# Kernel optimization log

Hardware: AMD Instinct MI355X
Metric: run time of the kernel (lower is better)

The kernel has to match this reference:

```python
import jax, jax.numpy as jnp
import numpy as np

EPS = 1e-7
LN_EPS = 1e-5

# Lorentz model, points represented by spatial coords x in R^dim; time coord t = sqrt(K + ||x||^2), K = 1/c.

def log_map_zero(x, c):
    K = 1.0 / c
    sqrtK = jnp.sqrt(K)
    xnorm = jnp.linalg.norm(x, axis=-1, keepdims=True)
    t = jnp.sqrt(K + xnorm * xnorm)
    theta = jnp.arccosh(jnp.maximum(t / sqrtK, 1.0 + EPS))
    return sqrtK * theta * x / jnp.maximum(xnorm, EPS)


def exp_map_zero(v, c):
    K = 1.0 / c
    sqrtK = jnp.sqrt(K)
    vnorm = jnp.linalg.norm(v, axis=-1, keepdims=True)
    return sqrtK * jnp.sinh(vnorm / sqrtK) * v / jnp.maximum(vnorm, EPS)


def layer_norm(x, gamma, beta):
    mu = jnp.mean(x, axis=-1, keepdims=True)
    var = jnp.mean((x - mu) ** 2, axis=-1, keepdims=True)
    return (x - mu) * jax.lax.rsqrt(var + LN_EPS) * gamma + beta


def setup_inputs() -> dict:
    key = jax.random.key(0)
    N, D, E, L = 50000, 128, 800000, 2
    ks = jax.random.split(key, 8)
    x_hyp = jax.random.normal(ks[0], (N, D), dtype=jnp.float32)
    edge_index = jax.random.randint(ks[1], (2, E), 0, N, dtype=jnp.int64)
    W = jax.random.normal(ks[2], (L, D, D), dtype=jnp.float32) / np.sqrt(D)
    b = jnp.zeros((L, D), dtype=jnp.float32)
    gamma = jnp.ones((L, D), dtype=jnp.float32)
    beta = jnp.zeros((L, D), dtype=jnp.float32)
    curv = jnp.ones((L,), dtype=jnp.float32)
    return {"x_hyp": x_hyp, "edge_index": edge_index, "W": W, "b": b,
            "gamma": gamma, "beta": beta, "curv": curv}


def reference(x_hyp, edge_index, W, b, gamma, beta, curv):
    N = x_hyp.shape[0]
    L = W.shape[0]
    src, dst = edge_index[0], edge_index[1]
    # in-degree counts for mean aggregation (clamped to avoid div by 0)
    counts = jax.ops.segment_sum(jnp.ones_like(dst, dtype=x_hyp.dtype), dst, num_segments=N)
    counts = jnp.maximum(counts, 1.0)[:, None]
    x = x_hyp
    for l in range(L):
        # curvature treated as constant (torch uses .item())
        c = jax.lax.stop_gradient(jnp.clip(curv[l], 0.1, 10.0))
        x_tan = log_map_zero(x, c)                      # [N, D]
        x_lin = x_tan @ W[l].T + b[l]                   # [N, D]
        msgs = x_lin[src]                               # [E, D] gather
        agg = jax.ops.segment_sum(msgs, dst, num_segments=N) / counts  # scatter-mean
        x_tan_out = layer_norm(x_tan + agg, gamma[l], beta[l])  # dropout in eval mode
        x = exp_map_zero(x_tan_out, c)
    return x
```

## Files before the change

kernel.cpp:

```cpp
#include <hip/hip_runtime.h>
#include <hip/hip_bf16.h>

typedef __attribute__((ext_vector_type(4))) float f32x4;
typedef __attribute__((ext_vector_type(8))) short bf16x8;

constexpr int D = 128;
constexpr int SB = 256;
constexpr int K4CAP = 8192;
#define FEPS 1e-7f
#define FLN_EPS 1e-5f

__device__ __forceinline__ float groupReduceSum16(float x) {
#pragma unroll
  for (int off = 1; off < 16; off <<= 1) x += __shfl_xor(x, off, 64);
  return x;
}

__device__ __forceinline__ unsigned short f2bf(float x) {
  unsigned int u = __float_as_uint(x);
  u += 0x7fffu + ((u >> 16) & 1u);
  return (unsigned short)(u >> 16);
}

__device__ __forceinline__ unsigned int pack2(float a, float b) {
  return (unsigned int)f2bf(a) | ((unsigned int)f2bf(b) << 16);
}

__device__ __forceinline__ void acc8(float* a, uint4 u) {
  a[0] += __uint_as_float(u.x << 16);
  a[1] += __uint_as_float(u.x & 0xffff0000u);
  a[2] += __uint_as_float(u.y << 16);
  a[3] += __uint_as_float(u.y & 0xffff0000u);
  a[4] += __uint_as_float(u.z << 16);
  a[5] += __uint_as_float(u.z & 0xffff0000u);
  a[6] += __uint_as_float(u.w << 16);
  a[7] += __uint_as_float(u.w & 0xffff0000u);
}


__global__ __launch_bounds__(1024) void k1_hist(const int* __restrict__ dst,
                                                int* __restrict__ bh, int E, int NB, int chunk) {
  __shared__ int h[256];
  int tid = threadIdx.x;
  if (tid < 256) h[tid] = 0;
  __syncthreads();
  int e0 = blockIdx.x * chunk;
  int e1 = min(e0 + chunk, E);
  for (int e = e0 + tid; e < e1; e += 1024) atomicAdd(&h[dst[e] >> 8], 1);
  __syncthreads();
  if (tid < NB) bh[tid * SB + blockIdx.x] = h[tid];
}

__global__ __launch_bounds__(1024) void k2_scan(int* __restrict__ bh,
                                                int* __restrict__ bucket_base, int NB, int E) {
  __shared__ int bsum[256];
  int tid = threadIdx.x, lane = tid & 63, wv = tid >> 6;
  for (int bin = wv; bin < NB; bin += 16) {
    int carry = 0;
    int* row = bh + bin * SB;
#pragma unroll
    for (int sgm = 0; sgm < 4; ++sgm) {
      int v = row[sgm * 64 + lane];
      int x = v;
#pragma unroll
      for (int off = 1; off < 64; off <<= 1) {
        int t = __shfl_up(x, off, 64);
        if (lane >= off) x += t;
      }
      row[sgm * 64 + lane] = carry + x - v;
      carry += __shfl(x, 63, 64);
    }
    if (lane == 0) bsum[bin] = carry;
  }
  __syncthreads();
  if (wv == 0) {
    int carry = 0;
    for (int base = 0; base < NB; base += 64) {
      int v = (base + lane < NB) ? bsum[base + lane] : 0;
      int x = v;
#pragma unroll
      for (int off = 1; off < 64; off <<= 1) {
        int t = __shfl_up(x, off, 64);
        if (lane >= off) x += t;
      }
      if (base + lane < NB) {
        int excl = carry + x - v;
        bsum[base + lane] = excl;
        bucket_base[base + lane] = excl;
      }
      carry += __shfl(x, 63, 64);
    }
    if (lane == 0) bucket_base[NB] = E;
  }
  __syncthreads();
  for (int bin = wv; bin < NB; bin += 16) {
    int bb = bsum[bin];
    int* row = bh + bin * SB;
    for (int s = lane; s < SB; s += 64) row[s] += bb;
  }
}

__global__ __launch_bounds__(1024) void k3_scatter(const int* __restrict__ src,
                                                   const int* __restrict__ dst,
                                                   const int* __restrict__ bh,
                                                   unsigned int* __restrict__ ebuf, int E,
                                                   int NB, int chunk) {
  __shared__ int base[256];
  __shared__ int cur[256];
  int tid = threadIdx.x;
  if (tid < 256) {
    base[tid] = (tid < NB) ? bh[tid * SB + blockIdx.x] : 0;
    cur[tid] = 0;
  }
  __syncthreads();
  int e0 = blockIdx.x * chunk;
  int e1 = min(e0 + chunk, E);
  for (int e = e0 + tid; e < e1; e += 1024) {
    int d = dst[e];
    int s = src[e];
    int bin = d >> 8;
    int r = atomicAdd(&cur[bin], 1);
    ebuf[base[bin] + r] = (unsigned int)(s & 0xffff) | ((unsigned int)(d & 255) << 16);
  }
}

__global__ __launch_bounds__(1024) void k4_csr(const unsigned int* __restrict__ ebuf,
                                               const int* __restrict__ bucket_base,
                                               int* __restrict__ rowptr,
                                               unsigned short* __restrict__ col, int N, int NB,
                                               int E) {
  __shared__ unsigned int stash[K4CAP];
  __shared__ int hist[256];
  __shared__ int cur[256];
  int b = blockIdx.x, tid = threadIdx.x;
  int e0 = bucket_base[b], e1 = bucket_base[b + 1];
  int cnt = e1 - e0;
  if (tid < 256) {
    hist[tid] = 0;
    cur[tid] = 0;
  }
  __syncthreads();
  for (int i = tid; i < cnt; i += 1024) {
    unsigned int u = ebuf[e0 + i];
    if (i < K4CAP) stash[i] = u;
    atomicAdd(&hist[u >> 16], 1);
  }
  __syncthreads();
  int lane = tid & 63;
  if (tid < 64) {
    int carry = 0;
#pragma unroll
    for (int sgm = 0; sgm < 4; ++sgm) {
      int v = hist[sgm * 64 + lane];
      int x = v;
#pragma unroll
      for (int off = 1; off < 64; off <<= 1) {
        int t = __shfl_up(x, off, 64);
        if (lane >= off) x += t;
      }
      hist[sgm * 64 + lane] = carry + x - v;
      carry += __shfl(x, 63, 64);
    }
  }
  __syncthreads();
  int node0 = b << 8;
  if (tid < 256 && node0 + tid < N) rowptr[node0 + tid] = e0 + hist[tid];
  if (b == 0 && tid == 0) rowptr[N] = E;
  for (int i = tid; i < cnt; i += 1024) {
    unsigned int u = (i < K4CAP) ? stash[i] : ebuf[e0 + i];
    int slot = u >> 16;
    int r = atomicAdd(&cur[slot], 1);
    col[e0 + hist[slot] + r] = (unsigned short)(u & 0xffff);
  }
}


template <int FIRST>
__global__ __launch_bounds__(256) void gemm_kernel(const float* __restrict__ xf,
                                                   const unsigned short* __restrict__ A,
                                                   const float* __restrict__ Wf,
                                                   const float* __restrict__ bias,
                                                   const float* __restrict__ curv, int l,
                                                   unsigned short* __restrict__ xt,
                                                   unsigned short* __restrict__ xl, int N) {
  __shared__ unsigned short Wlds[128 * 128];
  const float* Wp = Wf + (size_t)l * D * D;
  for (int idx = threadIdx.x; idx < 2048; idx += 256) {
    int lanei = idx & 63, kbt = idx >> 6;
    int kb = kbt & 3, tcol = kbt >> 2;
    int g = lanei >> 4, r = lanei & 15;
    const float* s = Wp + (size_t)(tcol * 16 + r) * D + kb * 32 + g * 8;
    float4 f0 = *reinterpret_cast<const float4*>(s);
    float4 f1 = *reinterpret_cast<const float4*>(s + 4);
    uint4 u;
    u.x = pack2(f0.x, f0.y);
    u.y = pack2(f0.z, f0.w);
    u.z = pack2(f1.x, f1.y);
    u.w = pack2(f1.z, f1.w);
    *reinterpret_cast<uint4*>(&Wlds[idx * 8]) = u;
  }
  __syncthreads();
  int lane = threadIdx.x & 63;
  int trow = blockIdx.x * 4 + (threadIdx.x >> 6);
  int n0 = trow * 16;
  if (n0 >= N) return;
  int g = lane >> 4, r = lane & 15;
  int ar = n0 + r;
  if (ar > N - 1) ar = N - 1;

  bf16x8 af[4];
  if (FIRST) {
    float c = fminf(fmaxf(curv[l], 0.1f), 10.0f);
    float K = 1.0f / c, sqrtK = sqrtf(K);
    float4 fa[4][2];
    float ss = 0.f;
#pragma unroll
    for (int kb = 0; kb < 4; ++kb) {
      const float4* xr = reinterpret_cast<const float4*>(xf + (size_t)ar * D + kb * 32 + g * 8);
      fa[kb][0] = xr[0];
      fa[kb][1] = xr[1];
      ss += fa[kb][0].x * fa[kb][0].x + fa[kb][0].y * fa[kb][0].y +
            fa[kb][0].z * fa[kb][0].z + fa[kb][0].w * fa[kb][0].w;
      ss += fa[kb][1].x * fa[kb][1].x + fa[kb][1].y * fa[kb][1].y +
            fa[kb][1].z * fa[kb][1].z + fa[kb][1].w * fa[kb][1].w;
    }
    ss += __shfl_xor(ss, 16, 64);
    ss += __shfl_xor(ss, 32, 64);
    float xnorm = sqrtf(ss);
    float t = sqrtf(K + ss);
    float theta = acoshf(fmaxf(t / sqrtK, 1.0f + FEPS));
    float scale = sqrtK * theta / fmaxf(xnorm, FEPS);
#pragma unroll
    for (int kb = 0; kb < 4; ++kb) {
      union { bf16x8 v; uint4 u; } cv;
      cv.u.x = pack2(fa[kb][0].x * scale, fa[kb][0].y * scale);
      cv.u.y = pack2(fa[kb][0].z * scale, fa[kb][0].w * scale);
      cv.u.z = pack2(fa[kb][1].x * scale, fa[kb][1].y * scale);
      cv.u.w = pack2(fa[kb][1].z * scale, fa[kb][1].w * scale);
      af[kb] = cv.v;
      *reinterpret_cast<uint4*>(xt + (size_t)ar * D + kb * 32 + g * 8) = cv.u;
    }
  } else {
#pragma unroll
    for (int kb = 0; kb < 4; ++kb)
      af[kb] = *reinterpret_cast<const bf16x8*>(A + (size_t)ar * D + kb * 32 + g * 8);
  }

  int colj = lane & 15, rb = (lane >> 4) * 4;
#pragma unroll
  for (int tcol = 0; tcol < 8; ++tcol) {
    f32x4 acc = {0.f, 0.f, 0.f, 0.f};
#pragma unroll
    for (int kb = 0; kb < 4; ++kb) {
      bf16x8 bfm = *reinterpret_cast<const bf16x8*>(&Wlds[((tcol * 4 + kb) * 64 + lane) * 8]);
      acc = __builtin_amdgcn_mfma_f32_16x16x32_bf16(af[kb], bfm, acc, 0, 0, 0);
    }
    float bv = bias[l * D + tcol * 16 + colj];
#pragma unroll
    for (int i = 0; i < 4; ++i) {
      int row = n0 + rb + i;
      if (row < N) xl[(size_t)row * D + tcol * 16 + colj] = f2bf(acc[i] + bv);
    }
  }
}


template <int MODE>
__global__ __launch_bounds__(256) void agg_kernel(const unsigned short* __restrict__ xl,
                                                  unsigned short* __restrict__ xt,
                                                  const int* __restrict__ rowptr,
                                                  const unsigned short* __restrict__ col,
                                                  const float* __restrict__ gamma,
                                                  const float* __restrict__ beta,
                                                  const float* __restrict__ curv, int l,
                                                  float* __restrict__ out, int N) {
  int tid = threadIdx.x;
  int lane = tid & 63;
  int gl = lane & 15, g = lane >> 4;
  int wid = tid >> 6;
  int node = blockIdx.x * 16 + wid * 4 + g;
  bool active = node < N;
  int nd = active ? node : N - 1;

  float c = fminf(fmaxf(curv[l], 0.1f), 10.0f);
  float K = 1.0f / c, sqrtK = sqrtf(K);

  int e0 = rowptr[nd], e1 = rowptr[nd + 1];
  int deg = e1 - e0;
  const unsigned short* cb = col + e0;

  float a[8], a2[8], a3[8], a4[8];
#pragma unroll
  for (int j = 0; j < 8; ++j) { a[j] = 0.f; a2[j] = 0.f; a3[j] = 0.f; a4[j] = 0.f; }

  const uint4* xlp = reinterpret_cast<const uint4*>(xl);
  for (int base = 0; base < deg; base += 16) {
    int cidx = (base + gl < deg) ? (int)cb[base + gl] : 0;
    int m = deg - base;
    if (m > 16) m = 16;
    int k = 0;
    for (; k + 4 <= m; k += 4) {
      int s0 = __shfl(cidx, g * 16 + k, 64);
      int s1 = __shfl(cidx, g * 16 + k + 1, 64);
      int s2 = __shfl(cidx, g * 16 + k + 2, 64);
      int s3 = __shfl(cidx, g * 16 + k + 3, 64);
      uint4 u0 = xlp[(size_t)s0 * 16 + gl];
      uint4 u1 = xlp[(size_t)s1 * 16 + gl];
      uint4 u2 = xlp[(size_t)s2 * 16 + gl];
      uint4 u3 = xlp[(size_t)s3 * 16 + gl];
      acc8(a, u0);
      acc8(a2, u1);
      acc8(a3, u2);
      acc8(a4, u3);
    }
    for (; k < m; ++k) {
      int s0 = __shfl(cidx, g * 16 + k, 64);
      uint4 u0 = xlp[(size_t)s0 * 16 + gl];
      acc8(a, u0);
    }
  }
#pragma unroll
  for (int j = 0; j < 8; ++j) a[j] += a2[j] + a3[j] + a4[j];

  float inv = 1.f / fmaxf((float)deg, 1.f);
  uint4 ut = reinterpret_cast<const uint4*>(xt)[(size_t)nd * 16 + gl];
  float v[8];
  v[0] = __uint_as_float(ut.x << 16) + a[0] * inv;
  v[1] = __uint_as_float(ut.x & 0xffff0000u) + a[1] * inv;
  v[2] = __uint_as_float(ut.y << 16) + a[2] * inv;
  v[3] = __uint_as_float(ut.y & 0xffff0000u) + a[3] * inv;
  v[4] = __uint_as_float(ut.z << 16) + a[4] * inv;
  v[5] = __uint_as_float(ut.z & 0xffff0000u) + a[5] * inv;
  v[6] = __uint_as_float(ut.w << 16) + a[6] * inv;
  v[7] = __uint_as_float(ut.w & 0xffff0000u) + a[7] * inv;

  float s1 = 0.f, s2 = 0.f;
#pragma unroll
  for (int j = 0; j < 8; ++j) { s1 += v[j]; s2 += v[j] * v[j]; }
  s1 = groupReduceSum16(s1);
  s2 = groupReduceSum16(s2);
  float mu = s1 * (1.f / 128.f);
  float var = fmaxf(s2 * (1.f / 128.f) - mu * mu, 0.f);
  float rstd = rsqrtf(var + FLN_EPS);

  float4 gm0 = *reinterpret_cast<const float4*>(gamma + l * D + gl * 8);
  float4 gm1 = *reinterpret_cast<const float4*>(gamma + l * D + gl * 8 + 4);
  float4 bt0 = *reinterpret_cast<const float4*>(beta + l * D + gl * 8);
  float4 bt1 = *reinterpret_cast<const float4*>(beta + l * D + gl * 8 + 4);
  float y[8];
  y[0] = (v[0] - mu) * rstd * gm0.x + bt0.x;
  y[1] = (v[1] - mu) * rstd * gm0.y + bt0.y;
  y[2] = (v[2] - mu) * rstd * gm0.z + bt0.z;
  y[3] = (v[3] - mu) * rstd * gm0.w + bt0.w;
  y[4] = (v[4] - mu) * rstd * gm1.x + bt1.x;
  y[5] = (v[5] - mu) * rstd * gm1.y + bt1.y;
  y[6] = (v[6] - mu) * rstd * gm1.z + bt1.z;
  y[7] = (v[7] - mu) * rstd * gm1.w + bt1.w;

  float ss = 0.f;
#pragma unroll
  for (int j = 0; j < 8; ++j) ss += y[j] * y[j];
  ss = groupReduceSum16(ss);
  float vn = sqrtf(ss);
  float sc = sqrtK * sinhf(vn / sqrtK) / fmaxf(vn, FEPS);

  if (MODE == 0) {
    if (active) {
      float4 o0, o1;
      o0.x = y[0] * sc; o0.y = y[1] * sc; o0.z = y[2] * sc; o0.w = y[3] * sc;
      o1.x = y[4] * sc; o1.y = y[5] * sc; o1.z = y[6] * sc; o1.w = y[7] * sc;
      float4* op = reinterpret_cast<float4*>(out + (size_t)node * D + gl * 8);
      op[0] = o0;
      op[1] = o1;
    }
  } else {
    float xn = sqrtK * sinhf(vn / sqrtK);
    float c2 = fminf(fmaxf(curv[l + 1], 0.1f), 10.0f);
    float K2 = 1.0f / c2, sqrtK2 = sqrtf(K2);
    float t2 = sqrtf(K2 + xn * xn);
    float theta = acoshf(fmaxf(t2 / sqrtK2, 1.0f + FEPS));
    float sc2 = sqrtK2 * theta / fmaxf(xn, FEPS);
    float st = sc * sc2;
    if (active) {
      uint4 w;
      w.x = pack2(y[0] * st, y[1] * st);
      w.y = pack2(y[2] * st, y[3] * st);
      w.z = pack2(y[4] * st, y[5] * st);
      w.w = pack2(y[6] * st, y[7] * st);
      reinterpret_cast<uint4*>(xt)[(size_t)node * 16 + gl] = w;
    }
  }
}


extern "C" void kernel_launch(void* const* d_in, const int* in_sizes, int n_in,
                              void* d_out, int out_size, void* d_ws, size_t ws_size,
                              hipStream_t stream) {
  const float* x_hyp = (const float*)d_in[0];
  const int* edge = (const int*)d_in[1];
  const float* W = (const float*)d_in[2];
  const float* b = (const float*)d_in[3];
  const float* gamma = (const float*)d_in[4];
  const float* beta = (const float*)d_in[5];
  const float* curv = (const float*)d_in[6];
  float* out = (float*)d_out;
  int N = in_sizes[0] / D;
  int E = in_sizes[1] / 2;
  int L = in_sizes[6];
  const int* src = edge;
  const int* dst = edge + E;

  char* p = (char*)d_ws;
  auto alloc = [&](size_t bytes) {
    char* r = p;
    p += (bytes + 255) & ~(size_t)255;
    return r;
  };
  int NB = (N + 255) >> 8;
  int chunk = (E + SB - 1) / SB;

  int* bh = (int*)alloc((size_t)256 * SB * 4);
  int* bucket_base = (int*)alloc((size_t)(NB + 1) * 4);
  unsigned int* ebuf = (unsigned int*)alloc((size_t)E * 4);
  int* rowptr = (int*)alloc((size_t)(N + 1) * 4);
  unsigned short* colp = (unsigned short*)alloc((size_t)E * 2);
  unsigned short* xt16 = (unsigned short*)alloc((size_t)N * D * 2);
  unsigned short* xl16 = (unsigned short*)alloc((size_t)N * D * 2);

  k1_hist<<<SB, 1024, 0, stream>>>(dst, bh, E, NB, chunk);
  k2_scan<<<1, 1024, 0, stream>>>(bh, bucket_base, NB, E);
  k3_scatter<<<SB, 1024, 0, stream>>>(src, dst, bh, ebuf, E, NB, chunk);
  k4_csr<<<NB, 1024, 0, stream>>>(ebuf, bucket_base, rowptr, colp, N, NB, E);

  int gblocks = ((N + 15) / 16 + 3) / 4;
  for (int l = 0; l < L; ++l) {
    if (l == 0) {
      gemm_kernel<1><<<gblocks, 256, 0, stream>>>(x_hyp, nullptr, W, b, curv, l, xt16, xl16, N);
    } else {
      gemm_kernel<0><<<gblocks, 256, 0, stream>>>(nullptr, xt16, W, b, curv, l, nullptr, xl16, N);
    }
    if (l < L - 1) {
      agg_kernel<1><<<(N + 15) / 16, 256, 0, stream>>>(xl16, xt16, rowptr, colp, gamma, beta,
                                                       curv, l, out, N);
    } else {
      agg_kernel<0><<<(N + 15) / 16, 256, 0, stream>>>(xl16, xt16, rowptr, colp, gamma, beta,
                                                       curv, l, out, N);
    }
  }
}
```

Measured before the change: 163.1 us.

## Fuse degree histogram with layer-0 GEMM and widen agg gather unroll

The first histogram kernel and the layer-0 projection GEMM now run as one launch. Blocks below SB build the histogram, reusing the LDS weight buffer as scratch, and the remaining blocks run the GEMM, so the two independent stages overlap and one launch is dropped. GEMM blocks grow from 256 to 1024 threads covering 16 row tiles each, which cuts how often each block converts and loads W into LDS. The aggregation loop now issues 8 gathers per iteration into packed float2 accumulators, aiming for more loads in flight and packed adds, at the cost of more registers and possibly lower occupancy.

```diff
diff --git a/kernel.cpp b/kernel.cpp
--- a/kernel.cpp
+++ b/kernel.cpp
@@ -2,6 +2,7 @@
 #include <hip/hip_bf16.h>
 
 typedef __attribute__((ext_vector_type(4))) float f32x4;
+typedef __attribute__((ext_vector_type(2))) float f32x2;
 typedef __attribute__((ext_vector_type(8))) short bf16x8;
 
 constexpr int D = 128;
@@ -26,30 +27,20 @@
   return (unsigned int)f2bf(a) | ((unsigned int)f2bf(b) << 16);
 }
 
-__device__ __forceinline__ void acc8(float* a, uint4 u) {
-  a[0] += __uint_as_float(u.x << 16);
-  a[1] += __uint_as_float(u.x & 0xffff0000u);
-  a[2] += __uint_as_float(u.y << 16);
-  a[3] += __uint_as_float(u.y & 0xffff0000u);
-  a[4] += __uint_as_float(u.z << 16);
-  a[5] += __uint_as_float(u.z & 0xffff0000u);
-  a[6] += __uint_as_float(u.w << 16);
-  a[7] += __uint_as_float(u.w & 0xffff0000u);
-}
-
-
-__global__ __launch_bounds__(1024) void k1_hist(const int* __restrict__ dst,
-                                                int* __restrict__ bh, int E, int NB, int chunk) {
-  __shared__ int h[256];
-  int tid = threadIdx.x;
-  if (tid < 256) h[tid] = 0;
-  __syncthreads();
-  int e0 = blockIdx.x * chunk;
-  int e1 = min(e0 + chunk, E);
-  for (int e = e0 + tid; e < e1; e += 1024) atomicAdd(&h[dst[e] >> 8], 1);
-  __syncthreads();
-  if (tid < NB) bh[tid * SB + blockIdx.x] = h[tid];
-}
+__device__ __forceinline__ f32x2 unp(unsigned int x) {
+  f32x2 r;
+  r.x = __uint_as_float(x << 16);
+  r.y = __uint_as_float(x & 0xffff0000u);
+  return r;
+}
+
+__device__ __forceinline__ void accp(f32x2* A, uint4 u) {
+  A[0] += unp(u.x);
+  A[1] += unp(u.y);
+  A[2] += unp(u.z);
+  A[3] += unp(u.w);
+}
+
 
 __global__ __launch_bounds__(1024) void k2_scan(int* __restrict__ bh,
                                                 int* __restrict__ bucket_base, int NB, int E) {
@@ -176,16 +167,16 @@
 
 
 template <int FIRST>
-__global__ __launch_bounds__(256) void gemm_kernel(const float* __restrict__ xf,
-                                                   const unsigned short* __restrict__ A,
-                                                   const float* __restrict__ Wf,
-                                                   const float* __restrict__ bias,
-                                                   const float* __restrict__ curv, int l,
-                                                   unsigned short* __restrict__ xt,
-                                                   unsigned short* __restrict__ xl, int N) {
-  __shared__ unsigned short Wlds[128 * 128];
+__device__ __forceinline__ void gemm_body1024(int gbid, unsigned short* Wlds,
+                                              const float* __restrict__ xf,
+                                              const unsigned short* __restrict__ A,
+                                              const float* __restrict__ Wf,
+                                              const float* __restrict__ bias,
+                                              const float* __restrict__ curv, int l,
+                                              unsigned short* __restrict__ xt,
+                                              unsigned short* __restrict__ xl, int N) {
   const float* Wp = Wf + (size_t)l * D * D;
-  for (int idx = threadIdx.x; idx < 2048; idx += 256) {
+  for (int idx = threadIdx.x; idx < 2048; idx += 1024) {
     int lanei = idx & 63, kbt = idx >> 6;
     int kb = kbt & 3, tcol = kbt >> 2;
     int g = lanei >> 4, r = lanei & 15;
@@ -201,7 +192,7 @@
   }
   __syncthreads();
   int lane = threadIdx.x & 63;
-  int trow = blockIdx.x * 4 + (threadIdx.x >> 6);
+  int trow = gbid * 16 + (threadIdx.x >> 6);
   int n0 = trow * 16;
   if (n0 >= N) return;
   int g = lane >> 4, r = lane & 15;
@@ -262,6 +253,40 @@
       if (row < N) xl[(size_t)row * D + tcol * 16 + colj] = f2bf(acc[i] + bv);
     }
   }
+}
+
+__global__ __launch_bounds__(1024) void fusedA_kernel(const int* __restrict__ dst,
+                                                      int* __restrict__ bh, int E, int NB,
+                                                      int chunk, const float* __restrict__ xf,
+                                                      const float* __restrict__ Wf,
+                                                      const float* __restrict__ bias,
+                                                      const float* __restrict__ curv,
+                                                      unsigned short* __restrict__ xt,
+                                                      unsigned short* __restrict__ xl, int N) {
+  __shared__ unsigned short Wlds[128 * 128];
+  int bid = blockIdx.x;
+  if (bid < SB) {
+    int* h = (int*)Wlds;
+    int tid = threadIdx.x;
+    if (tid < 256) h[tid] = 0;
+    __syncthreads();
+    int e0 = bid * chunk;
+    int e1 = min(e0 + chunk, E);
+    for (int e = e0 + tid; e < e1; e += 1024) atomicAdd(&h[dst[e] >> 8], 1);
+    __syncthreads();
+    if (tid < NB) bh[tid * SB + bid] = h[tid];
+  } else {
+    gemm_body1024<1>(bid - SB, Wlds, xf, nullptr, Wf, bias, curv, 0, xt, xl, N);
+  }
+}
+
+__global__ __launch_bounds__(1024) void gemm_kernel(const unsigned short* __restrict__ A,
+                                                    const float* __restrict__ Wf,
+                                                    const float* __restrict__ bias,
+                                                    const float* __restrict__ curv, int l,
+                                                    unsigned short* __restrict__ xl, int N) {
+  __shared__ unsigned short Wlds[128 * 128];
+  gemm_body1024<0>(blockIdx.x, Wlds, nullptr, A, Wf, bias, curv, l, nullptr, xl, N);
 }
 
 
@@ -289,9 +314,14 @@
   int deg = e1 - e0;
   const unsigned short* cb = col + e0;
 
-  float a[8], a2[8], a3[8], a4[8];
-#pragma unroll
-  for (int j = 0; j < 8; ++j) { a[j] = 0.f; a2[j] = 0.f; a3[j] = 0.f; a4[j] = 0.f; }
+  f32x2 A0[4], A1[4], A2[4], A3[4];
+#pragma unroll
+  for (int j = 0; j < 4; ++j) {
+    A0[j] = 0.f;
+    A1[j] = 0.f;
+    A2[j] = 0.f;
+    A3[j] = 0.f;
+  }
 
   const uint4* xlp = reinterpret_cast<const uint4*>(xl);
   for (int base = 0; base < deg; base += 16) {
@@ -299,40 +329,53 @@
     int m = deg - base;
     if (m > 16) m = 16;
     int k = 0;
-    for (; k + 4 <= m; k += 4) {
+    for (; k + 8 <= m; k += 8) {
+      uint4 u[8];
+#pragma unroll
+      for (int t = 0; t < 8; ++t) {
+        int s = __shfl(cidx, g * 16 + k + t, 64);
+        u[t] = xlp[(size_t)s * 16 + gl];
+      }
+      accp(A0, u[0]);
+      accp(A1, u[1]);
+      accp(A2, u[2]);
+      accp(A3, u[3]);
+      accp(A0, u[4]);
+      accp(A1, u[5]);
+      accp(A2, u[6]);
+      accp(A3, u[7]);
+    }
+    for (; k + 2 <= m; k += 2) {
       int s0 = __shfl(cidx, g * 16 + k, 64);
       int s1 = __shfl(cidx, g * 16 + k + 1, 64);
-      int s2 = __shfl(cidx, g * 16 + k + 2, 64);
-      int s3 = __shfl(cidx, g * 16 + k + 3, 64);
       uint4 u0 = xlp[(size_t)s0 * 16 + gl];
       uint4 u1 = xlp[(size_t)s1 * 16 + gl];
-      uint4 u2 = xlp[(size_t)s2 * 16 + gl];
-      uint4 u3 = xlp[(size_t)s3 * 16 + gl];
-      acc8(a, u0);
-      acc8(a2, u1);
-      acc8(a3, u2);
-      acc8(a4, u3);
-    }
-    for (; k < m; ++k) {
+      accp(A0, u0);
+      accp(A1, u1);
+    }
+    if (k < m) {
       int s0 = __shfl(cidx, g * 16 + k, 64);
       uint4 u0 = xlp[(size_t)s0 * 16 + gl];
-      acc8(a, u0);
-    }
-  }
-#pragma unroll
-  for (int j = 0; j < 8; ++j) a[j] += a2[j] + a3[j] + a4[j];
+      accp(A0, u0);
+    }
+  }
+  f32x2 AV[4];
+#pragma unroll
+  for (int j = 0; j < 4; ++j) AV[j] = (A0[j] + A1[j]) + (A2[j] + A3[j]);
 
   float inv = 1.f / fmaxf((float)deg, 1.f);
   uint4 ut = reinterpret_cast<const uint4*>(xt)[(size_t)nd * 16 + gl];
+  f32x2 utv[4];
+  utv[0] = unp(ut.x);
+  utv[1] = unp(ut.y);
+  utv[2] = unp(ut.z);
+  utv[3] = unp(ut.w);
   float v[8];
-  v[0] = __uint_as_float(ut.x << 16) + a[0] * inv;
-  v[1] = __uint_as_float(ut.x & 0xffff0000u) + a[1] * inv;
-  v[2] = __uint_as_float(ut.y << 16) + a[2] * inv;
-  v[3] = __uint_as_float(ut.y & 0xffff0000u) + a[3] * inv;
-  v[4] = __uint_as_float(ut.z << 16) + a[4] * inv;
-  v[5] = __uint_as_float(ut.z & 0xffff0000u) + a[5] * inv;
-  v[6] = __uint_as_float(ut.w << 16) + a[6] * inv;
-  v[7] = __uint_as_float(ut.w & 0xffff0000u) + a[7] * inv;
+#pragma unroll
+  for (int j = 0; j < 4; ++j) {
+    v[2 * j] = utv[j].x + AV[j].x * inv;
+    v[2 * j + 1] = utv[j].y + AV[j].y * inv;
+  }
 
   float s1 = 0.f, s2 = 0.f;
 #pragma unroll
@@ -427,17 +470,17 @@
   unsigned short* xt16 = (unsigned short*)alloc((size_t)N * D * 2);
   unsigned short* xl16 = (unsigned short*)alloc((size_t)N * D * 2);
 
-  k1_hist<<<SB, 1024, 0, stream>>>(dst, bh, E, NB, chunk);
+  int g1024 = ((N + 15) / 16 + 15) / 16;
+
+  fusedA_kernel<<<SB + g1024, 1024, 0, stream>>>(dst, bh, E, NB, chunk, x_hyp, W, b, curv,
+                                                 xt16, xl16, N);
   k2_scan<<<1, 1024, 0, stream>>>(bh, bucket_base, NB, E);
   k3_scatter<<<SB, 1024, 0, stream>>>(src, dst, bh, ebuf, E, NB, chunk);
   k4_csr<<<NB, 1024, 0, stream>>>(ebuf, bucket_base, rowptr, colp, N, NB, E);
 
-  int gblocks = ((N + 15) / 16 + 3) / 4;
   for (int l = 0; l < L; ++l) {
-    if (l == 0) {
-      gemm_kernel<1><<<gblocks, 256, 0, stream>>>(x_hyp, nullptr, W, b, curv, l, xt16, xl16, N);
-    } else {
-      gemm_kernel<0><<<gblocks, 256, 0, stream>>>(nullptr, xt16, W, b, curv, l, nullptr, xl16, N);
+    if (l > 0) {
+      gemm_kernel<<<g1024, 1024, 0, stream>>>(xt16, W, b, curv, l, xl16, N);
     }
     if (l < L - 1) {
       agg_kernel<1><<<(N + 15) / 16, 256, 0, stream>>>(xl16, xt16, rowptr, colp, gamma, beta,
```

Result: faster. 151.4 us (-7.1%).
